# Kernel tuning notes

Hardware: AMD Instinct MI355X
Metric: run time of the kernel (lower is better)

Reference implementation:

```python
import jax, jax.numpy as jnp
import numpy as np

DIM = 2048
N_HEADS = 16
N_KV_HEADS = 4
HEAD_DIM = 128
EPS = 1e-6
BS, SEQ = 2, 4096


def setup_inputs() -> dict:
    key = jax.random.key(0)
    ks = jax.random.split(key, 8)
    x = jax.random.normal(ks[0], (BS, SEQ, DIM), dtype=jnp.float32)
    # rotary freqs: unit-modulus complex represented as [seq, head_dim//2, 2]
    theta = 10000.0
    inv_freq = 1.0 / (theta ** (jnp.arange(0, HEAD_DIM, 2, dtype=jnp.float32) / HEAD_DIM))
    t = jnp.arange(SEQ, dtype=jnp.float32)
    ang = jnp.outer(t, inv_freq)  # [SEQ, HEAD_DIM//2]
    freqs_cis = jnp.stack([jnp.cos(ang), jnp.sin(ang)], axis=-1)  # [SEQ, HD/2, 2]
    std = 0.02
    wq = jax.random.normal(ks[1], (N_HEADS * HEAD_DIM, DIM), dtype=jnp.float32) * std
    wk = jax.random.normal(ks[2], (N_KV_HEADS * HEAD_DIM, DIM), dtype=jnp.float32) * std
    wv = jax.random.normal(ks[3], (N_KV_HEADS * HEAD_DIM, DIM), dtype=jnp.float32) * std
    wo = jax.random.normal(ks[4], (DIM, N_HEADS * HEAD_DIM), dtype=jnp.float32) * std
    q_norm_w = jnp.ones((HEAD_DIM,), dtype=jnp.float32)
    k_norm_w = jnp.ones((HEAD_DIM,), dtype=jnp.float32)
    return {"x": x, "freqs_cis": freqs_cis, "wq": wq, "wk": wk, "wv": wv,
            "wo": wo, "q_norm_w": q_norm_w, "k_norm_w": k_norm_w}


def _rms_norm(x, w, eps=EPS):
    xf = x.astype(jnp.float32)
    var = jnp.mean(xf * xf, axis=-1, keepdims=True)
    return w * (xf * jax.lax.rsqrt(var + eps)).astype(x.dtype)


def _apply_rope(x, freqs_cis):
    # x: [b, s, h, d]; freqs_cis: [s, d//2, 2] (cos, sin)
    b, s, h, d = x.shape
    xr = x.astype(jnp.float32).reshape(b, s, h, d // 2, 2)
    cos = freqs_cis[:s, :, 0][None, :, None, :]
    sin = freqs_cis[:s, :, 1][None, :, None, :]
    xre, xim = xr[..., 0], xr[..., 1]
    out = jnp.stack([xre * cos - xim * sin, xre * sin + xim * cos], axis=-1)
    return out.reshape(b, s, h, d).astype(x.dtype)


def reference(x, freqs_cis, wq, wk, wv, wo, q_norm_w, k_norm_w):
    bs, seqlen, _ = x.shape
    xq = jnp.einsum('bsd,ed->bse', x, wq).reshape(bs, seqlen, N_HEADS, HEAD_DIM)
    xk = jnp.einsum('bsd,ed->bse', x, wk).reshape(bs, seqlen, N_KV_HEADS, HEAD_DIM)
    xv = jnp.einsum('bsd,ed->bse', x, wv).reshape(bs, seqlen, N_KV_HEADS, HEAD_DIM)
    xq = _rms_norm(xq, q_norm_w)
    xk = _rms_norm(xk, k_norm_w)
    xq = _apply_rope(xq, freqs_cis)
    xk = _apply_rope(xk, freqs_cis)
    n_rep = N_HEADS // N_KV_HEADS
    # repeat_kv: [b,s,kvh,d] -> [b,s,kvh*n_rep,d]
    keys = jnp.repeat(xk, n_rep, axis=2)
    values = jnp.repeat(xv, n_rep, axis=2)
    q = xq.transpose(0, 2, 1, 3)  # [b,h,s,d]
    k = keys.transpose(0, 2, 1, 3)
    v = values.transpose(0, 2, 1, 3)
    scale = 1.0 / jnp.sqrt(jnp.asarray(HEAD_DIM, dtype=q.dtype))
    scores = jnp.einsum('bhqd,bhkd->bhqk', q, k) * scale
    causal = jnp.tril(jnp.ones((seqlen, seqlen), dtype=bool))
    scores = jnp.where(causal[None, None], scores, jnp.finfo(scores.dtype).min)
    attn = jax.nn.softmax(scores, axis=-1)
    out = jnp.einsum('bhqk,bhkd->bhqd', attn, v)
    out = out.transpose(0, 2, 1, 3).reshape(bs, seqlen, N_HEADS * HEAD_DIM)
    return jnp.einsum('bse,de->bsd', out, wo)
```

## Files before the change

kernel.cpp:

```cpp
#include <hip/hip_runtime.h>

typedef __bf16 bf16;
typedef __bf16 bf16x8 __attribute__((ext_vector_type(8)));
typedef __bf16 bf16x4 __attribute__((ext_vector_type(4)));
typedef __bf16 bf16x2 __attribute__((ext_vector_type(2)));
typedef float  f32x4  __attribute__((ext_vector_type(4)));

static_assert(sizeof(bf16x8) == 16, "bf16x8 must be 16B");

#define MFMA16(a, b, c) __builtin_amdgcn_mfma_f32_16x16x32_bf16((a), (b), (c), 0, 0, 0)

__device__ __forceinline__ void gload_lds16(const void* g, void* l) {
    __builtin_amdgcn_global_load_lds(
        (const __attribute__((address_space(1))) void*)(uintptr_t)g,
        (__attribute__((address_space(3))) void*)(uintptr_t)l,
        16, 0, 0);
}

__global__ __launch_bounds__(256)
void cast_f32_bf16(const float* __restrict__ in, bf16* __restrict__ out, int n8)
{
    const int i = blockIdx.x * 256 + threadIdx.x;
    if (i >= n8) return;
    const float4 a = ((const float4*)in)[i * 2];
    const float4 b = ((const float4*)in)[i * 2 + 1];
    bf16x8 o;
    o[0] = (bf16)a.x; o[1] = (bf16)a.y; o[2] = (bf16)a.z; o[3] = (bf16)a.w;
    o[4] = (bf16)b.x; o[5] = (bf16)b.y; o[6] = (bf16)b.z; o[7] = (bf16)b.w;
    ((bf16x8*)out)[i] = o;
}

template <typename OT>
__global__ __launch_bounds__(256)
void gemm_bt(const bf16* __restrict__ A, const bf16* __restrict__ W,
             int K, int ldc, OT* __restrict__ C)
{
    __shared__ bf16 As[128 * 32];
    __shared__ bf16 Bs[128 * 32];

    const int n0 = blockIdx.x * 128;
    const int m0 = blockIdx.y * 128;

    const int tid  = threadIdx.x;
    const int lane = tid & 63;
    const int wid  = tid >> 6;
    const int wm   = wid >> 1;
    const int wn   = wid & 1;
    const int quad = lane >> 4;
    const int l16  = lane & 15;

    const int srow = wid * 32 + (lane >> 2);
    const int scol = (lane & 3) * 8;
    const bf16* ag = A + (size_t)(m0 + srow) * K + scol;
    const bf16* wg = W + (size_t)(n0 + srow) * K + scol;
    bf16* al = As + wid * 1024;
    bf16* bl = Bs + wid * 1024;

    const bf16* afr = As + (wm * 64 + l16) * 32 + quad * 8;
    const bf16* bfr = Bs + (wn * 64 + l16) * 32 + quad * 8;

    f32x4 acc[4][4];
#pragma unroll
    for (int i = 0; i < 4; i++)
#pragma unroll
        for (int j = 0; j < 4; j++) acc[i][j] = f32x4{0.f, 0.f, 0.f, 0.f};

    for (int kt = 0; kt < K; kt += 32) {
        __syncthreads();
        gload_lds16(ag,          al);
        gload_lds16(ag + 16 * K, al + 512);
        gload_lds16(wg,          bl);
        gload_lds16(wg + 16 * K, bl + 512);
        ag += 32; wg += 32;
        __syncthreads();

        bf16x8 af[4], bfv[4];
#pragma unroll
        for (int i = 0; i < 4; i++) af[i]  = *(const bf16x8*)(afr + i * 16 * 32);
#pragma unroll
        for (int i = 0; i < 4; i++) bfv[i] = *(const bf16x8*)(bfr + i * 16 * 32);
#pragma unroll
        for (int mi = 0; mi < 4; mi++)
#pragma unroll
            for (int ni = 0; ni < 4; ni++)
                acc[mi][ni] = MFMA16(af[mi], bfv[ni], acc[mi][ni]);
    }

#pragma unroll
    for (int mi = 0; mi < 4; mi++) {
        const int row = m0 + wm * 64 + mi * 16 + quad * 4;
#pragma unroll
        for (int ni = 0; ni < 4; ni++) {
            const int col = n0 + wn * 64 + ni * 16 + l16;
#pragma unroll
            for (int r = 0; r < 4; r++)
                C[(size_t)(row + r) * ldc + col] = (OT)acc[mi][ni][r];
        }
    }
}

__global__ __launch_bounds__(256)
void normrope(bf16* __restrict__ qkv, const float* __restrict__ fc,
              const float* __restrict__ qw, const float* __restrict__ kw)
{
    const int row  = blockIdx.x * 4 + (threadIdx.x >> 6);
    const int lane = threadIdx.x & 63;
    const int slot = row % 20;
    const int tok  = row / 20;
    const int s    = tok & 4095;

    const float* w; int off; float post;
    if (slot < 16) { off = slot * 128;               w = qw; post = 0.12751681555f; }
    else           { off = 2048 + (slot - 16) * 128; w = kw; post = 1.0f; }

    bf16* p = qkv + (size_t)tok * 3072 + off;

    bf16x2 v = *(const bf16x2*)(p + 2 * lane);
    float x0 = (float)v[0], x1 = (float)v[1];

    float ss = x0 * x0 + x1 * x1;
    ss += __shfl_xor(ss, 1);  ss += __shfl_xor(ss, 2);  ss += __shfl_xor(ss, 4);
    ss += __shfl_xor(ss, 8);  ss += __shfl_xor(ss, 16); ss += __shfl_xor(ss, 32);
    const float r = rsqrtf(ss * (1.0f / 128.0f) + 1e-6f) * post;

    const float xn0 = x0 * r * w[2 * lane], xn1 = x1 * r * w[2 * lane + 1];

    const float2 cs = ((const float2*)fc)[(size_t)s * 64 + lane];
    const float c = cs.x, sn = cs.y;

    bf16x2 o;
    o[0] = (bf16)(xn0 * c - xn1 * sn);
    o[1] = (bf16)(xn0 * sn + xn1 * c);
    *(bf16x2*)(p + 2 * lane) = o;
}

__global__ __launch_bounds__(256)
void transpose_v(const bf16* __restrict__ qkv, bf16* __restrict__ vT)
{
    __shared__ bf16 T[64][130];
    const int st = blockIdx.x;
    const int bk = blockIdx.y;
    const int b = bk >> 2, kvh = bk & 3;
    const int w = threadIdx.x >> 6, lane = threadIdx.x & 63;
    const int s0 = st * 64;

    const bf16* src = qkv + (size_t)(b * 4096 + s0) * 3072 + 2560 + kvh * 128;
#pragma unroll
    for (int i = 0; i < 16; i++) {
        const int s = w * 16 + i;
        const bf16x2 v = *(const bf16x2*)(src + (size_t)s * 3072 + 2 * lane);
        *(bf16x2*)(&T[s][2 * lane]) = v;
    }
    __syncthreads();

    bf16* dst = vT + ((size_t)bk * 128) * 4096 + s0;
#pragma unroll
    for (int i = 0; i < 16; i++) {
        const int d = w * 32 + 2 * i + (lane >> 5);
        const int s = (lane & 31) * 2;
        bf16x2 o;
        o[0] = T[s][d];
        o[1] = T[s + 1][d];
        *(bf16x2*)(dst + (size_t)d * 4096 + s) = o;
    }
}

__global__ __launch_bounds__(256)
void flash(const bf16* __restrict__ qkv, const bf16* __restrict__ vT,
           bf16* __restrict__ out)
{
    const int bh  = blockIdx.y;
    const int b   = bh >> 4, h = bh & 15;
    const int kvh = h >> 2;

    const int tid  = threadIdx.x;
    const int lane = tid & 63;
    const int wid  = tid >> 6;
    const int quad = lane >> 4;
    const int l16  = lane & 15;
    const int key  = l16 & 7;

    __shared__ bf16 Ks[2][64 * 128];
    __shared__ bf16 Vs[128 * 64];
    __shared__ bf16 Ps[128 * 64];

    const bf16* kbase = qkv + (size_t)b * 4096 * 3072 + 2048 + kvh * 128;
    const bf16* vbase = vT + ((size_t)(b * 4 + kvh) * 128) * 4096;

    const int krow_off = lane >> 4;
    const int kcolg    = lane & 15;
    const int vrow_off = lane >> 3;
    const int vcolg    = lane & 7;

    bf16x8 vone;
#pragma unroll
    for (int j = 0; j < 8; j++) vone[j] = (bf16)1.0f;

    for (int pass = 0; pass < 2; ++pass) {
        const int qt = pass ? (31 - blockIdx.x) : blockIdx.x;
        const int q0 = qt * 128;
        const int ntiles = qt * 2 + 2;

        __syncthreads();
#pragma unroll
        for (int i = 0; i < 4; i++) {
            const int r0 = wid * 16 + i * 4;
            const int rk = r0 + krow_off;
            const int gc = (kcolg ^ (rk & 7)) * 8;
            gload_lds16(kbase + (size_t)rk * 3072 + gc, &Ks[0][r0 * 128]);
        }

        bf16x8 qf[2][4];
        const bf16* qbase = qkv + ((size_t)(b * 4096 + q0 + wid * 32)) * 3072 + h * 128;
#pragma unroll
        for (int mt = 0; mt < 2; mt++)
#pragma unroll
            for (int ks = 0; ks < 4; ks++)
                qf[mt][ks] = *(const bf16x8*)(qbase + (size_t)(mt * 16 + l16) * 3072 + ks * 32 + quad * 8);

        f32x4 oacc[2][8];
        f32x4 lacc[2];
#pragma unroll
        for (int mt = 0; mt < 2; mt++) {
#pragma unroll
            for (int nd = 0; nd < 8; nd++) oacc[mt][nd] = f32x4{0.f, 0.f, 0.f, 0.f};
            lacc[mt] = f32x4{0.f, 0.f, 0.f, 0.f};
        }
        float mrow[2];
#pragma unroll
        for (int mt = 0; mt < 2; mt++) mrow[mt] = -__builtin_inff();

        int cur = 0;
        for (int t = 0; t < ntiles; t++) {
            const int kv0 = t * 64;
            __syncthreads();

#pragma unroll
            for (int i = 0; i < 4; i++) {
                const int r0 = wid * 32 + i * 8;
                const int dv = r0 + vrow_off;
                const int gc = (vcolg ^ (dv & 7)) * 8;
                gload_lds16(vbase + (size_t)dv * 4096 + kv0 + gc, &Vs[r0 * 64]);
            }
            if (t + 1 < ntiles) {
                const int kvn = kv0 + 64;
#pragma unroll
                for (int i = 0; i < 4; i++) {
                    const int r0 = wid * 16 + i * 4;
                    const int rk = r0 + krow_off;
                    const int gc = (kcolg ^ (rk & 7)) * 8;
                    gload_lds16(kbase + (size_t)(kvn + rk) * 3072 + gc, &Ks[1 - cur][r0 * 128]);
                }
            }

            f32x4 sacc[2][4];
#pragma unroll
            for (int mt = 0; mt < 2; mt++)
#pragma unroll
                for (int nt = 0; nt < 4; nt++) sacc[mt][nt] = f32x4{0.f, 0.f, 0.f, 0.f};
            __builtin_amdgcn_s_setprio(1);
#pragma unroll
            for (int ks = 0; ks < 4; ks++) {
                bf16x8 kf[4];
#pragma unroll
                for (int nt = 0; nt < 4; nt++)
                    kf[nt] = *(const bf16x8*)(&Ks[cur][(nt * 16 + l16) * 128 + (((ks * 4 + quad) ^ key) * 8)]);
#pragma unroll
                for (int mt = 0; mt < 2; mt++)
#pragma unroll
                    for (int nt = 0; nt < 4; nt++)
                        sacc[mt][nt] = MFMA16(kf[nt], qf[mt][ks], sacc[mt][nt]);
            }
            __builtin_amdgcn_s_setprio(0);

            if (kv0 + 63 > q0) {
#pragma unroll
                for (int mt = 0; mt < 2; mt++) {
                    const int qg = q0 + wid * 32 + mt * 16 + l16;
#pragma unroll
                    for (int nt = 0; nt < 4; nt++)
#pragma unroll
                        for (int r = 0; r < 4; r++) {
                            const int kvg = kv0 + nt * 16 + quad * 4 + r;
                            if (kvg > qg) sacc[mt][nt][r] = -1e30f;
                        }
                }
            }

            float pm[2];
#pragma unroll
            for (int mt = 0; mt < 2; mt++) {
                float t8[8];
#pragma unroll
                for (int nt = 0; nt < 4; nt++) {
                    t8[2 * nt]     = fmaxf(sacc[mt][nt][0], sacc[mt][nt][1]);
                    t8[2 * nt + 1] = fmaxf(sacc[mt][nt][2], sacc[mt][nt][3]);
                }
                float m = fmaxf(fmaxf(fmaxf(t8[0], t8[1]), fmaxf(t8[2], t8[3])),
                                fmaxf(fmaxf(t8[4], t8[5]), fmaxf(t8[6], t8[7])));
                m = fmaxf(m, __shfl_xor(m, 16));
                m = fmaxf(m, __shfl_xor(m, 32));
                pm[mt] = m;
            }

            const bool rescale =
                !__all((pm[0] - mrow[0] <= 8.f) && (pm[1] - mrow[1] <= 8.f));
            if (rescale) {
#pragma unroll
                for (int mt = 0; mt < 2; mt++) {
                    const float mnew  = fmaxf(mrow[mt], pm[mt]);
                    const float alpha = exp2f(mrow[mt] - mnew);
                    mrow[mt] = mnew;
                    float ar[4];
#pragma unroll
                    for (int r = 0; r < 4; r++) ar[r] = __shfl(alpha, quad * 4 + r);
#pragma unroll
                    for (int nd = 0; nd < 8; nd++)
#pragma unroll
                        for (int r = 0; r < 4; r++) oacc[mt][nd][r] *= ar[r];
#pragma unroll
                    for (int r = 0; r < 4; r++) lacc[mt][r] *= ar[r];
                }
            }

#pragma unroll
            for (int mt = 0; mt < 2; mt++) {
                const int prow = wid * 32 + mt * 16 + l16;
#pragma unroll
                for (int nt = 0; nt < 4; nt++) {
                    const float p0 = exp2f(sacc[mt][nt][0] - mrow[mt]);
                    const float p1 = exp2f(sacc[mt][nt][1] - mrow[mt]);
                    const float p2 = exp2f(sacc[mt][nt][2] - mrow[mt]);
                    const float p3 = exp2f(sacc[mt][nt][3] - mrow[mt]);
                    bf16x4 h4;
                    h4[0] = (bf16)p0; h4[1] = (bf16)p1;
                    h4[2] = (bf16)p2; h4[3] = (bf16)p3;
                    const int g = (2 * nt + (quad >> 1)) ^ key;
                    *(bf16x4*)(&Ps[prow * 64 + g * 8 + (quad & 1) * 4]) = h4;
                }
            }

            __syncthreads();

            __builtin_amdgcn_s_setprio(1);
#pragma unroll
            for (int ks = 0; ks < 2; ks++) {
                bf16x8 pf[2];
#pragma unroll
                for (int mt = 0; mt < 2; mt++)
                    pf[mt] = *(const bf16x8*)(&Ps[(wid * 32 + mt * 16 + l16) * 64 + (((ks * 4 + quad) ^ key) * 8)]);
#pragma unroll
                for (int nd = 0; nd < 8; nd++) {
                    const bf16x8 vf = *(const bf16x8*)(&Vs[(nd * 16 + l16) * 64 + (((ks * 4 + quad) ^ key) * 8)]);
#pragma unroll
                    for (int mt = 0; mt < 2; mt++)
                        oacc[mt][nd] = MFMA16(pf[mt], vf, oacc[mt][nd]);
                }
#pragma unroll
                for (int mt = 0; mt < 2; mt++)
                    lacc[mt] = MFMA16(pf[mt], vone, lacc[mt]);
            }
            __builtin_amdgcn_s_setprio(0);
            cur ^= 1;
        }

#pragma unroll
        for (int mt = 0; mt < 2; mt++) {
#pragma unroll
            for (int r = 0; r < 4; r++) {
                const float inv = 1.0f / lacc[mt][r];
                const size_t srow = (size_t)(b * 4096 + q0 + wid * 32 + mt * 16 + quad * 4 + r);
#pragma unroll
                for (int nd = 0; nd < 8; nd++)
                    out[srow * 2048 + h * 128 + nd * 16 + l16] = (bf16)(oacc[mt][nd][r] * inv);
            }
        }
    }
}

extern "C" void kernel_launch(void* const* d_in, const int* in_sizes, int n_in,
                              void* d_out, int out_size, void* d_ws, size_t ws_size,
                              hipStream_t stream)
{
    const float* x   = (const float*)d_in[0];
    const float* fc  = (const float*)d_in[1];
    const float* wq  = (const float*)d_in[2];
    const float* wk  = (const float*)d_in[3];
    const float* wv  = (const float*)d_in[4];
    const float* wo  = (const float*)d_in[5];
    const float* qnw = (const float*)d_in[6];
    const float* knw = (const float*)d_in[7];
    float* out = (float*)d_out;

    char* ws = (char*)d_ws;
    bf16* qkv = (bf16*)ws;
    bf16* vT  = (bf16*)(ws + 50331648);
    bf16* xb  = (bf16*)(ws + 58720256);
    bf16* att = xb;
    bf16* wb  = (bf16*)(ws + 92274688);
    bf16* wob = wb;

    cast_f32_bf16<<<dim3(8192), 256, 0, stream>>>(x, xb, 2097152);
    cast_f32_bf16<<<dim3(2048), 256, 0, stream>>>(wq, wb, 524288);
    cast_f32_bf16<<<dim3(512),  256, 0, stream>>>(wk, wb + 2048 * 2048, 131072);
    cast_f32_bf16<<<dim3(512),  256, 0, stream>>>(wv, wb + 2560 * 2048, 131072);
    gemm_bt<bf16><<<dim3(24, 64), 256, 0, stream>>>(xb, wb, 2048, 3072, qkv);
    normrope<<<dim3(40960), 256, 0, stream>>>(qkv, fc, qnw, knw);
    transpose_v<<<dim3(64, 8), 256, 0, stream>>>(qkv, vT);
    flash<<<dim3(16, 32), 256, 0, stream>>>(qkv, vT, att);
    cast_f32_bf16<<<dim3(2048), 256, 0, stream>>>(wo, wob, 524288);
    gemm_bt<float><<<dim3(16, 64), 256, 0, stream>>>(att, wob, 2048, 2048, out);
}
```

Measured before the change: 686.6 us.

## Software-pipeline QK^T of next tile with PV in flash attention

Restructures the flash attention loop so the QK^T MFMAs for tile t+1 are issued between the softmax and the PV MFMAs of tile t, using ping-pong score registers and a two-step unrolled loop. V and next-K loads are moved to the end of each step behind an extra barrier. The row-sum is now computed with scalar adds and shuffles instead of an extra MFMA against a ones vector. Launch bounds request two blocks per CU, which adds register pressure from the duplicated score accumulators and may cause spills.

```diff
diff --git a/kernel.cpp b/kernel.cpp
--- a/kernel.cpp
+++ b/kernel.cpp
@@ -165,7 +165,7 @@
     }
 }
 
-__global__ __launch_bounds__(256)
+__global__ __launch_bounds__(256, 2)
 void flash(const bf16* __restrict__ qkv, const bf16* __restrict__ vT,
            bf16* __restrict__ out)
 {
@@ -192,10 +192,6 @@
     const int vrow_off = lane >> 3;
     const int vcolg    = lane & 7;
 
-    bf16x8 vone;
-#pragma unroll
-    for (int j = 0; j < 8; j++) vone[j] = (bf16)1.0f;
-
     for (int pass = 0; pass < 2; ++pass) {
         const int qt = pass ? (31 - blockIdx.x) : blockIdx.x;
         const int q0 = qt * 128;
@@ -219,59 +215,56 @@
                 qf[mt][ks] = *(const bf16x8*)(qbase + (size_t)(mt * 16 + l16) * 3072 + ks * 32 + quad * 8);
 
         f32x4 oacc[2][8];
-        f32x4 lacc[2];
-#pragma unroll
-        for (int mt = 0; mt < 2; mt++) {
+#pragma unroll
+        for (int mt = 0; mt < 2; mt++)
 #pragma unroll
             for (int nd = 0; nd < 8; nd++) oacc[mt][nd] = f32x4{0.f, 0.f, 0.f, 0.f};
-            lacc[mt] = f32x4{0.f, 0.f, 0.f, 0.f};
-        }
-        float mrow[2];
-#pragma unroll
-        for (int mt = 0; mt < 2; mt++) mrow[mt] = -__builtin_inff();
-
-        int cur = 0;
-        for (int t = 0; t < ntiles; t++) {
-            const int kv0 = t * 64;
-            __syncthreads();
-
-#pragma unroll
-            for (int i = 0; i < 4; i++) {
-                const int r0 = wid * 32 + i * 8;
-                const int dv = r0 + vrow_off;
-                const int gc = (vcolg ^ (dv & 7)) * 8;
-                gload_lds16(vbase + (size_t)dv * 4096 + kv0 + gc, &Vs[r0 * 64]);
-            }
-            if (t + 1 < ntiles) {
-                const int kvn = kv0 + 64;
-#pragma unroll
-                for (int i = 0; i < 4; i++) {
-                    const int r0 = wid * 16 + i * 4;
-                    const int rk = r0 + krow_off;
-                    const int gc = (kcolg ^ (rk & 7)) * 8;
-                    gload_lds16(kbase + (size_t)(kvn + rk) * 3072 + gc, &Ks[1 - cur][r0 * 128]);
-                }
-            }
-
-            f32x4 sacc[2][4];
+        float mrow[2], lrow[2];
+#pragma unroll
+        for (int mt = 0; mt < 2; mt++) { mrow[mt] = -__builtin_inff(); lrow[mt] = 0.f; }
+
+        __syncthreads();
+
+#pragma unroll
+        for (int i = 0; i < 4; i++) {
+            const int r0 = wid * 32 + i * 8;
+            const int dv = r0 + vrow_off;
+            const int gc = (vcolg ^ (dv & 7)) * 8;
+            gload_lds16(vbase + (size_t)dv * 4096 + gc, &Vs[r0 * 64]);
+        }
+#pragma unroll
+        for (int i = 0; i < 4; i++) {
+            const int r0 = wid * 16 + i * 4;
+            const int rk = r0 + krow_off;
+            const int gc = (kcolg ^ (rk & 7)) * 8;
+            gload_lds16(kbase + (size_t)(64 + rk) * 3072 + gc, &Ks[1][r0 * 128]);
+        }
+
+        f32x4 sA[2][4], sB[2][4];
+
+        {
 #pragma unroll
             for (int mt = 0; mt < 2; mt++)
 #pragma unroll
-                for (int nt = 0; nt < 4; nt++) sacc[mt][nt] = f32x4{0.f, 0.f, 0.f, 0.f};
+                for (int nt = 0; nt < 4; nt++) sA[mt][nt] = f32x4{0.f, 0.f, 0.f, 0.f};
             __builtin_amdgcn_s_setprio(1);
 #pragma unroll
             for (int ks = 0; ks < 4; ks++) {
                 bf16x8 kf[4];
 #pragma unroll
                 for (int nt = 0; nt < 4; nt++)
-                    kf[nt] = *(const bf16x8*)(&Ks[cur][(nt * 16 + l16) * 128 + (((ks * 4 + quad) ^ key) * 8)]);
+                    kf[nt] = *(const bf16x8*)(&Ks[0][(nt * 16 + l16) * 128 + (((ks * 4 + quad) ^ key) * 8)]);
 #pragma unroll
                 for (int mt = 0; mt < 2; mt++)
 #pragma unroll
                     for (int nt = 0; nt < 4; nt++)
-                        sacc[mt][nt] = MFMA16(kf[nt], qf[mt][ks], sacc[mt][nt]);
+                        sA[mt][nt] = MFMA16(kf[nt], qf[mt][ks], sA[mt][nt]);
             }
             __builtin_amdgcn_s_setprio(0);
+        }
+
+        auto step = [&](int t, f32x4 (&SA)[2][4], f32x4 (&SB)[2][4]) {
+            const int kv0 = t * 64;
 
             if (kv0 + 63 > q0) {
 #pragma unroll
@@ -282,7 +275,7 @@
 #pragma unroll
                         for (int r = 0; r < 4; r++) {
                             const int kvg = kv0 + nt * 16 + quad * 4 + r;
-                            if (kvg > qg) sacc[mt][nt][r] = -1e30f;
+                            if (kvg > qg) SA[mt][nt][r] = -1e30f;
                         }
                 }
             }
@@ -293,8 +286,8 @@
                 float t8[8];
 #pragma unroll
                 for (int nt = 0; nt < 4; nt++) {
-                    t8[2 * nt]     = fmaxf(sacc[mt][nt][0], sacc[mt][nt][1]);
-                    t8[2 * nt + 1] = fmaxf(sacc[mt][nt][2], sacc[mt][nt][3]);
+                    t8[2 * nt]     = fmaxf(SA[mt][nt][0], SA[mt][nt][1]);
+                    t8[2 * nt + 1] = fmaxf(SA[mt][nt][2], SA[mt][nt][3]);
                 }
                 float m = fmaxf(fmaxf(fmaxf(t8[0], t8[1]), fmaxf(t8[2], t8[3])),
                                 fmaxf(fmaxf(t8[4], t8[5]), fmaxf(t8[6], t8[7])));
@@ -311,6 +304,7 @@
                     const float mnew  = fmaxf(mrow[mt], pm[mt]);
                     const float alpha = exp2f(mrow[mt] - mnew);
                     mrow[mt] = mnew;
+                    lrow[mt] *= alpha;
                     float ar[4];
 #pragma unroll
                     for (int r = 0; r < 4; r++) ar[r] = __shfl(alpha, quad * 4 + r);
@@ -318,29 +312,54 @@
                     for (int nd = 0; nd < 8; nd++)
 #pragma unroll
                         for (int r = 0; r < 4; r++) oacc[mt][nd][r] *= ar[r];
-#pragma unroll
-                    for (int r = 0; r < 4; r++) lacc[mt][r] *= ar[r];
                 }
             }
 
 #pragma unroll
             for (int mt = 0; mt < 2; mt++) {
                 const int prow = wid * 32 + mt * 16 + l16;
+                float sn[4];
 #pragma unroll
                 for (int nt = 0; nt < 4; nt++) {
-                    const float p0 = exp2f(sacc[mt][nt][0] - mrow[mt]);
-                    const float p1 = exp2f(sacc[mt][nt][1] - mrow[mt]);
-                    const float p2 = exp2f(sacc[mt][nt][2] - mrow[mt]);
-                    const float p3 = exp2f(sacc[mt][nt][3] - mrow[mt]);
+                    const float p0 = exp2f(SA[mt][nt][0] - mrow[mt]);
+                    const float p1 = exp2f(SA[mt][nt][1] - mrow[mt]);
+                    const float p2 = exp2f(SA[mt][nt][2] - mrow[mt]);
+                    const float p3 = exp2f(SA[mt][nt][3] - mrow[mt]);
+                    sn[nt] = (p0 + p1) + (p2 + p3);
                     bf16x4 h4;
                     h4[0] = (bf16)p0; h4[1] = (bf16)p1;
                     h4[2] = (bf16)p2; h4[3] = (bf16)p3;
                     const int g = (2 * nt + (quad >> 1)) ^ key;
                     *(bf16x4*)(&Ps[prow * 64 + g * 8 + (quad & 1) * 4]) = h4;
                 }
+                float s = (sn[0] + sn[1]) + (sn[2] + sn[3]);
+                s += __shfl_xor(s, 16);
+                s += __shfl_xor(s, 32);
+                lrow[mt] += s;
             }
 
             __syncthreads();
+
+            if (t + 1 < ntiles) {
+#pragma unroll
+                for (int mt = 0; mt < 2; mt++)
+#pragma unroll
+                    for (int nt = 0; nt < 4; nt++) SB[mt][nt] = f32x4{0.f, 0.f, 0.f, 0.f};
+                __builtin_amdgcn_s_setprio(1);
+#pragma unroll
+                for (int ks = 0; ks < 4; ks++) {
+                    bf16x8 kf[4];
+#pragma unroll
+                    for (int nt = 0; nt < 4; nt++)
+                        kf[nt] = *(const bf16x8*)(&Ks[(t + 1) & 1][(nt * 16 + l16) * 128 + (((ks * 4 + quad) ^ key) * 8)]);
+#pragma unroll
+                    for (int mt = 0; mt < 2; mt++)
+#pragma unroll
+                        for (int nt = 0; nt < 4; nt++)
+                            SB[mt][nt] = MFMA16(kf[nt], qf[mt][ks], SB[mt][nt]);
+                }
+                __builtin_amdgcn_s_setprio(0);
+            }
 
             __builtin_amdgcn_s_setprio(1);
 #pragma unroll
@@ -356,23 +375,49 @@
                     for (int mt = 0; mt < 2; mt++)
                         oacc[mt][nd] = MFMA16(pf[mt], vf, oacc[mt][nd]);
                 }
-#pragma unroll
-                for (int mt = 0; mt < 2; mt++)
-                    lacc[mt] = MFMA16(pf[mt], vone, lacc[mt]);
             }
             __builtin_amdgcn_s_setprio(0);
-            cur ^= 1;
+
+            if (t + 1 < ntiles) {
+                __syncthreads();
+                const int kvv = (t + 1) * 64;
+#pragma unroll
+                for (int i = 0; i < 4; i++) {
+                    const int r0 = wid * 32 + i * 8;
+                    const int dv = r0 + vrow_off;
+                    const int gc = (vcolg ^ (dv & 7)) * 8;
+                    gload_lds16(vbase + (size_t)dv * 4096 + kvv + gc, &Vs[r0 * 64]);
+                }
+                if (t + 2 < ntiles) {
+                    const int kvn = (t + 2) * 64;
+#pragma unroll
+                    for (int i = 0; i < 4; i++) {
+                        const int r0 = wid * 16 + i * 4;
+                        const int rk = r0 + krow_off;
+                        const int gc = (kcolg ^ (rk & 7)) * 8;
+                        gload_lds16(kbase + (size_t)(kvn + rk) * 3072 + gc, &Ks[t & 1][r0 * 128]);
+                    }
+                }
+            }
+        };
+
+        for (int t = 0; t < ntiles; t += 2) {
+            step(t,     sA, sB);
+            step(t + 1, sB, sA);
         }
 
 #pragma unroll
         for (int mt = 0; mt < 2; mt++) {
+            const float inv = 1.0f / lrow[mt];
+            float invr[4];
+#pragma unroll
+            for (int r = 0; r < 4; r++) invr[r] = __shfl(inv, quad * 4 + r);
 #pragma unroll
             for (int r = 0; r < 4; r++) {
-                const float inv = 1.0f / lacc[mt][r];
                 const size_t srow = (size_t)(b * 4096 + q0 + wid * 32 + mt * 16 + quad * 4 + r);
 #pragma unroll
                 for (int nd = 0; nd < 8; nd++)
-                    out[srow * 2048 + h * 128 + nd * 16 + l16] = (bf16)(oacc[mt][nd][r] * inv);
+                    out[srow * 2048 + h * 128 + nd * 16 + l16] = (bf16)(oacc[mt][nd][r] * invr[r]);
             }
         }
     }
```

Result: faster. 651.5 us (-5.1%).
